# Kernel tuning notes

Measured on AMD Instinct MI355X. Metric: run time of the kernel, lower is better.

## Reference

```python
import jax, jax.numpy as jnp
import numpy as np

SCALE = 2

def pixel_shuffle(x, r):
    # x: (B, C*r*r, H, W) -> (B, C, H*r, W*r), torch F.pixel_shuffle ordering
    B, C, H, W = x.shape
    Co = C // (r * r)
    x = x.reshape(B, Co, r, r, H, W)
    x = x.transpose(0, 1, 4, 2, 5, 3)  # (B, Co, H, r, W, r)
    return x.reshape(B, Co, H * r, W * r)

def grid_sample_bilinear_zeros(x, grid):
    # x: (B,C,H,W); grid: (B,Ho,Wo,2), grid[...,0]=x-coord, grid[...,1]=y-coord
    # mode='bilinear', padding_mode='zeros', align_corners=False
    B, C, H, W = x.shape
    ix = ((grid[..., 0] + 1.0) * W - 1.0) * 0.5
    iy = ((grid[..., 1] + 1.0) * H - 1.0) * 0.5
    ix0 = jnp.floor(ix)
    iy0 = jnp.floor(iy)
    wx1 = ix - ix0
    wy1 = iy - iy0
    img = x.transpose(0, 2, 3, 1)  # (B,H,W,C) for channel-contiguous gathers
    b = jnp.arange(B)[:, None, None]

    def corner(iy_, ix_, w):
        valid = (ix_ >= 0) & (ix_ < W) & (iy_ >= 0) & (iy_ < H)
        ic = jnp.clip(ix_, 0, W - 1).astype(jnp.int32)
        jc = jnp.clip(iy_, 0, H - 1).astype(jnp.int32)
        v = img[b, jc, ic]  # (B,Ho,Wo,C)
        return v * (w * valid)[..., None]

    out = (corner(iy0, ix0, (1 - wy1) * (1 - wx1))
           + corner(iy0, ix0 + 1, (1 - wy1) * wx1)
           + corner(iy0 + 1, ix0, wy1 * (1 - wx1))
           + corner(iy0 + 1, ix0 + 1, wy1 * wx1))
    return out.transpose(0, 3, 1, 2)  # (B,C,Ho,Wo)

def setup_inputs() -> dict:
    key = jax.random.key(0)
    k1, k2, k3 = jax.random.split(key, 3)
    B, C, H, W = 16, 256, 64, 64
    x = jax.random.normal(k1, (B, C, H, W), dtype=jnp.float32)
    # 1x1 conv: weight (2*scale^2, C); original inits to zero, small random
    # values used here to exercise the learned-offset sampling path.
    weight = jax.random.normal(k2, (2 * SCALE * SCALE, C), dtype=jnp.float32) * 0.01
    bias = jax.random.normal(k3, (2 * SCALE * SCALE,), dtype=jnp.float32) * 0.01
    return {"x": x, "weight": weight, "bias": bias}

def reference(x, weight, bias):
    r = SCALE
    B, C, H, W = x.shape
    # 1x1 conv producing 2*r*r offset channels
    offset = jnp.einsum('bchw,oc->bohw', x, weight) + bias[None, :, None, None]
    offset = pixel_shuffle(offset, r)  # (B, 2, H*r, W*r)
    h_range = jnp.linspace(-1.0, 1.0, H * r, dtype=x.dtype)
    w_range = jnp.linspace(-1.0, 1.0, W * r, dtype=x.dtype)
    gh, gw = jnp.meshgrid(h_range, w_range, indexing='ij')
    # NOTE: original stacks (h, w) but grid_sample reads [...,0] as x-coord;
    # we reproduce that behavior exactly.
    grid = jnp.stack([gh, gw], axis=-1)[None]  # (1, Hr, Wr, 2)
    grid = grid + offset.transpose(0, 2, 3, 1)  # (B, Hr, Wr, 2)
    return grid_sample_bilinear_zeros(x, grid)
```

## Files before the change

### kernel.cpp

```cpp
#include <hip/hip_runtime.h>
#include <hip/hip_bf16.h>


#define NB 16
#define NC 256
#define NH 64
#define NW 64
#define NHO 128
#define NWO 128
#define PLANE (NH*NW)
#define OPLANE (NHO*NWO)

static __device__ __forceinline__ float bf2f(unsigned short u) {
    return __uint_as_float(((unsigned int)u) << 16);
}
static __device__ __forceinline__ unsigned short f2bf(float f) {
    unsigned int u = __float_as_uint(f);
    u = (u + 0x7FFFu + ((u >> 16) & 1u)) >> 16;
    return (unsigned short)u;
}
static __device__ __forceinline__ uint4 pack8(const float* r) {
    uint4 u;
    u.x = (unsigned)f2bf(r[0]) | ((unsigned)f2bf(r[1]) << 16);
    u.y = (unsigned)f2bf(r[2]) | ((unsigned)f2bf(r[3]) << 16);
    u.z = (unsigned)f2bf(r[4]) | ((unsigned)f2bf(r[5]) << 16);
    u.w = (unsigned)f2bf(r[6]) | ((unsigned)f2bf(r[7]) << 16);
    return u;
}

__global__ void k_detect(const unsigned int* __restrict__ xw, int* __restrict__ flag)
{
    __shared__ int cnt;
    if (threadIdx.x == 0) cnt = 0;
    __syncthreads();
    unsigned int w = xw[threadIdx.x];
    int el = (int)((w >> 7)  & 0xFFu);
    int eh = (int)((w >> 23) & 0xFFu);
    bool ok = (el >= 97 && el <= 143) && (eh >= 97 && eh <= 143);
    if (ok) atomicAdd(&cnt, 1);
    __syncthreads();
    if (threadIdx.x == 0) *flag = (cnt >= 192) ? 1 : 0;
}

__global__ __launch_bounds__(128) void k_offsets(
    const void* __restrict__ x_,
    const void* __restrict__ w_,
    const void* __restrict__ b_,
    float2* __restrict__ coords,
    const int* __restrict__ flag)
{
    __shared__ float4 wl4[NC * 2];
    float* wl = (float*)wl4;
    const int tid = threadIdx.x;
    const int isbf = *flag;

    if (isbf) {
        const unsigned short* weight = (const unsigned short*)w_;
        #pragma unroll
        for (int i = 0; i < 16; ++i) {
            int idx = tid * 16 + i;
            int c = idx >> 3, o = idx & 7;
            wl[idx] = bf2f(weight[o * NC + c]);
        }
    } else {
        const float* weight = (const float*)w_;
        #pragma unroll
        for (int i = 0; i < 16; ++i) {
            int idx = tid * 16 + i;
            int c = idx >> 3, o = idx & 7;
            wl[idx] = weight[o * NC + c];
        }
    }
    __syncthreads();

    float bv[8];
    if (isbf) {
        const unsigned short* bias = (const unsigned short*)b_;
        #pragma unroll
        for (int o = 0; o < 8; ++o) bv[o] = bf2f(bias[o]);
    } else {
        const float* bias = (const float*)b_;
        #pragma unroll
        for (int o = 0; o < 8; ++o) bv[o] = bias[o];
    }

    const int p0 = blockIdx.x * 256 + tid;
    const int p1 = p0 + 128;
    const int b0 = p0 >> 12, h0 = (p0 >> 6) & 63, w0 = p0 & 63;
    const int b1 = p1 >> 12, h1 = (p1 >> 6) & 63, w1 = p1 & 63;
    const size_t off0 = (size_t)b0 * NC * PLANE + h0 * NW + w0;
    const size_t off1 = (size_t)b1 * NC * PLANE + h1 * NW + w1;

    float a0[8], a1[8];
    #pragma unroll
    for (int o = 0; o < 8; ++o) { a0[o] = 0.0f; a1[o] = 0.0f; }

    if (isbf) {
        const unsigned short* xp0 = (const unsigned short*)x_ + off0;
        const unsigned short* xp1 = (const unsigned short*)x_ + off1;
        #pragma unroll 4
        for (int c = 0; c < NC; ++c) {
            float4 wA = wl4[c * 2], wB = wl4[c * 2 + 1];
            float wv[8] = { wA.x, wA.y, wA.z, wA.w, wB.x, wB.y, wB.z, wB.w };
            float xv0 = bf2f(xp0[c * PLANE]);
            float xv1 = bf2f(xp1[c * PLANE]);
            #pragma unroll
            for (int o = 0; o < 8; ++o) {
                a0[o] = fmaf(xv0, wv[o], a0[o]);
                a1[o] = fmaf(xv1, wv[o], a1[o]);
            }
        }
    } else {
        const float* xp0 = (const float*)x_ + off0;
        const float* xp1 = (const float*)x_ + off1;
        #pragma unroll 4
        for (int c = 0; c < NC; ++c) {
            float4 wA = wl4[c * 2], wB = wl4[c * 2 + 1];
            float wv[8] = { wA.x, wA.y, wA.z, wA.w, wB.x, wB.y, wB.z, wB.w };
            float xv0 = xp0[c * PLANE];
            float xv1 = xp1[c * PLANE];
            #pragma unroll
            for (int o = 0; o < 8; ++o) {
                a0[o] = fmaf(xv0, wv[o], a0[o]);
                a1[o] = fmaf(xv1, wv[o], a1[o]);
            }
        }
    }
    #pragma unroll
    for (int o = 0; o < 8; ++o) { a0[o] += bv[o]; a1[o] += bv[o]; }

    #pragma unroll
    for (int ry = 0; ry < 2; ++ry) {
        #pragma unroll
        for (int rx = 0; rx < 2; ++rx) {
            int q = ry * 2 + rx;
            {
                int ho = 2 * h0 + ry, wo = 2 * w0 + rx;
                float gh = fmaf((float)ho, 2.0f / 127.0f, -1.0f);
                float gw = fmaf((float)wo, 2.0f / 127.0f, -1.0f);
                float ix = ((gh + a0[q] + 1.0f) * 64.0f - 1.0f) * 0.5f;
                float iy = ((gw + a0[q + 4] + 1.0f) * 64.0f - 1.0f) * 0.5f;
                coords[(size_t)b0 * OPLANE + ho * NWO + wo] = make_float2(ix, iy);
            }
            {
                int ho = 2 * h1 + ry, wo = 2 * w1 + rx;
                float gh = fmaf((float)ho, 2.0f / 127.0f, -1.0f);
                float gw = fmaf((float)wo, 2.0f / 127.0f, -1.0f);
                float ix = ((gh + a1[q] + 1.0f) * 64.0f - 1.0f) * 0.5f;
                float iy = ((gw + a1[q + 4] + 1.0f) * 64.0f - 1.0f) * 0.5f;
                coords[(size_t)b1 * OPLANE + ho * NWO + wo] = make_float2(ix, iy);
            }
        }
    }
}

__global__ __launch_bounds__(256) void k_sample(
    const void* __restrict__ x_,
    const float2* __restrict__ coords,
    void* __restrict__ out_,
    const int* __restrict__ flag)
{
    __shared__ float4 plane[PLANE];
    const int tid = threadIdx.x;
    const int blk = blockIdx.x;
    const int g = blk & 63;
    const int b = blk >> 6;
    const int isbf = *flag;

    const size_t chbase = (size_t)(b * NC + g * 4) * PLANE;
    if (isbf) {
        const unsigned short* xb = (const unsigned short*)x_ + chbase;
        #pragma unroll
        for (int i = 0; i < 16; ++i) {
            int pos = i * 256 + tid;
            float4 v;
            v.x = bf2f(xb[pos]);
            v.y = bf2f(xb[PLANE + pos]);
            v.z = bf2f(xb[2 * PLANE + pos]);
            v.w = bf2f(xb[3 * PLANE + pos]);
            int y = pos >> 6;
            plane[(y << 6) | ((pos + (y >> 2)) & 63)] = v;
        }
    } else {
        const float* xb = (const float*)x_ + chbase;
        #pragma unroll
        for (int i = 0; i < 16; ++i) {
            int pos = i * 256 + tid;
            float4 v;
            v.x = xb[pos];
            v.y = xb[PLANE + pos];
            v.z = xb[2 * PLANE + pos];
            v.w = xb[3 * PLANE + pos];
            int y = pos >> 6;
            plane[(y << 6) | ((pos + (y >> 2)) & 63)] = v;
        }
    }
    __syncthreads();

    const float2* cb = coords + (size_t)b * OPLANE;
    const size_t obase = (size_t)(b * NC + g * 4) * OPLANE;

    #pragma unroll 1
    for (int it = 0; it < 8; ++it) {
        const int base = it * 2048 + tid * 8;
        float r0[8], r1[8], r2[8], r3[8];
        #pragma unroll
        for (int j = 0; j < 8; ++j) {
            float2 cd = cb[base + j];
            float ix = cd.x, iy = cd.y;
            float fx0 = floorf(ix), fy0 = floorf(iy);
            float wx1 = ix - fx0, wy1 = iy - fy0;
            float wx0 = 1.0f - wx1, wy0 = 1.0f - wy1;
            int x0 = (int)fx0, y0 = (int)fy0;
            int x1 = x0 + 1, y1 = y0 + 1;
            bool vx0 = (unsigned)x0 < 64u, vx1 = (unsigned)x1 < 64u;
            bool vy0 = (unsigned)y0 < 64u, vy1 = (unsigned)y1 < 64u;
            float w00 = (vy0 & vx0) ? wy0 * wx0 : 0.0f;
            float w01 = (vy0 & vx1) ? wy0 * wx1 : 0.0f;
            float w10 = (vy1 & vx0) ? wy1 * wx0 : 0.0f;
            float w11 = (vy1 & vx1) ? wy1 * wx1 : 0.0f;
            int x0c = min(max(x0, 0), 63), x1c = min(max(x1, 0), 63);
            int y0c = min(max(y0, 0), 63), y1c = min(max(y1, 0), 63);
            int ry0 = y0c >> 2, ry1 = y1c >> 2;
            float4 a00 = plane[(y0c << 6) | ((x0c + ry0) & 63)];
            float4 a01 = plane[(y0c << 6) | ((x1c + ry0) & 63)];
            float4 a10 = plane[(y1c << 6) | ((x0c + ry1) & 63)];
            float4 a11 = plane[(y1c << 6) | ((x1c + ry1) & 63)];
            r0[j] = w00 * a00.x + w01 * a01.x + w10 * a10.x + w11 * a11.x;
            r1[j] = w00 * a00.y + w01 * a01.y + w10 * a10.y + w11 * a11.y;
            r2[j] = w00 * a00.z + w01 * a01.z + w10 * a10.z + w11 * a11.z;
            r3[j] = w00 * a00.w + w01 * a01.w + w10 * a10.w + w11 * a11.w;
        }
        if (isbf) {
            unsigned short* ob = (unsigned short*)out_ + obase;
            *reinterpret_cast<uint4*>(ob + base)              = pack8(r0);
            *reinterpret_cast<uint4*>(ob + OPLANE + base)     = pack8(r1);
            *reinterpret_cast<uint4*>(ob + 2 * OPLANE + base) = pack8(r2);
            *reinterpret_cast<uint4*>(ob + 3 * OPLANE + base) = pack8(r3);
        } else {
            float* ob = (float*)out_ + obase;
            #pragma unroll
            for (int ch = 0; ch < 4; ++ch) {
                const float* rr = (ch == 0) ? r0 : (ch == 1) ? r1 : (ch == 2) ? r2 : r3;
                *reinterpret_cast<float4*>(ob + ch * OPLANE + base)     = make_float4(rr[0], rr[1], rr[2], rr[3]);
                *reinterpret_cast<float4*>(ob + ch * OPLANE + base + 4) = make_float4(rr[4], rr[5], rr[6], rr[7]);
            }
        }
    }
}

extern "C" void kernel_launch(void* const* d_in, const int* in_sizes, int n_in,
                              void* d_out, int out_size, void* d_ws, size_t ws_size,
                              hipStream_t stream)
{
    int* flag = (int*)d_ws;
    float2* coords = (float2*)((char*)d_ws + 256);

    hipLaunchKernelGGL(k_detect, dim3(1), dim3(256), 0, stream,
                       (const unsigned int*)d_in[0], flag);
    hipLaunchKernelGGL(k_offsets, dim3(256), dim3(128), 0, stream,
                       d_in[0], d_in[1], d_in[2], coords, flag);
    hipLaunchKernelGGL(k_sample, dim3(NB * 64), dim3(256), 0, stream,
                       d_in[0], coords, d_out, flag);
}
```

Baseline: 358.9 us.

## Drop dtype detection, split channel reduction across warps, widen sampling blocks

Removes the bf16 detection kernel and all bf16 branches, so x, weight and bias are assumed to be fp32. The offset conv now runs one block per output row, splits the 256 input channels across four waves and combines the partial sums in shared memory, then writes coordinates as float4. The sampling kernel goes to 512 threads, drops the LDS bank-swizzle, reads two coordinates per float4 and writes float2 outputs. This cuts a launch and raises parallelism in the conv, at the cost of possible LDS bank conflicts on the gathers and narrower output stores.

```diff
diff --git a/kernel.cpp b/kernel.cpp
--- a/kernel.cpp
+++ b/kernel.cpp
@@ -1,5 +1,4 @@
 #include <hip/hip_runtime.h>
-#include <hip/hip_bf16.h>
 
 
 #define NB 16
@@ -11,241 +10,145 @@
 #define PLANE (NH*NW)
 #define OPLANE (NHO*NWO)
 
-static __device__ __forceinline__ float bf2f(unsigned short u) {
-    return __uint_as_float(((unsigned int)u) << 16);
-}
-static __device__ __forceinline__ unsigned short f2bf(float f) {
-    unsigned int u = __float_as_uint(f);
-    u = (u + 0x7FFFu + ((u >> 16) & 1u)) >> 16;
-    return (unsigned short)u;
-}
-static __device__ __forceinline__ uint4 pack8(const float* r) {
-    uint4 u;
-    u.x = (unsigned)f2bf(r[0]) | ((unsigned)f2bf(r[1]) << 16);
-    u.y = (unsigned)f2bf(r[2]) | ((unsigned)f2bf(r[3]) << 16);
-    u.z = (unsigned)f2bf(r[4]) | ((unsigned)f2bf(r[5]) << 16);
-    u.w = (unsigned)f2bf(r[6]) | ((unsigned)f2bf(r[7]) << 16);
-    return u;
-}
-
-__global__ void k_detect(const unsigned int* __restrict__ xw, int* __restrict__ flag)
-{
-    __shared__ int cnt;
-    if (threadIdx.x == 0) cnt = 0;
-    __syncthreads();
-    unsigned int w = xw[threadIdx.x];
-    int el = (int)((w >> 7)  & 0xFFu);
-    int eh = (int)((w >> 23) & 0xFFu);
-    bool ok = (el >= 97 && el <= 143) && (eh >= 97 && eh <= 143);
-    if (ok) atomicAdd(&cnt, 1);
-    __syncthreads();
-    if (threadIdx.x == 0) *flag = (cnt >= 192) ? 1 : 0;
-}
-
-__global__ __launch_bounds__(128) void k_offsets(
-    const void* __restrict__ x_,
-    const void* __restrict__ w_,
-    const void* __restrict__ b_,
-    float2* __restrict__ coords,
-    const int* __restrict__ flag)
+__global__ __launch_bounds__(256, 4) void k_offsets(
+    const float* __restrict__ x,
+    const float* __restrict__ weight,
+    const float* __restrict__ bias,
+    float2* __restrict__ coords)
 {
     __shared__ float4 wl4[NC * 2];
+    __shared__ float red[4][64][8];
     float* wl = (float*)wl4;
     const int tid = threadIdx.x;
-    const int isbf = *flag;
+    const int qid = tid >> 6, w = tid & 63;
+    const int row = blockIdx.x;
+    const int b = row >> 6, h = row & 63;
 
-    if (isbf) {
-        const unsigned short* weight = (const unsigned short*)w_;
-        #pragma unroll
-        for (int i = 0; i < 16; ++i) {
-            int idx = tid * 16 + i;
-            int c = idx >> 3, o = idx & 7;
-            wl[idx] = bf2f(weight[o * NC + c]);
-        }
-    } else {
-        const float* weight = (const float*)w_;
-        #pragma unroll
-        for (int i = 0; i < 16; ++i) {
-            int idx = tid * 16 + i;
-            int c = idx >> 3, o = idx & 7;
-            wl[idx] = weight[o * NC + c];
-        }
+    #pragma unroll
+    for (int i = 0; i < 8; ++i) {
+        int idx = tid * 8 + i;
+        wl[idx] = weight[(idx & 7) * NC + (idx >> 3)];
     }
     __syncthreads();
 
-    float bv[8];
-    if (isbf) {
-        const unsigned short* bias = (const unsigned short*)b_;
-        #pragma unroll
-        for (int o = 0; o < 8; ++o) bv[o] = bf2f(bias[o]);
-    } else {
-        const float* bias = (const float*)b_;
-        #pragma unroll
-        for (int o = 0; o < 8; ++o) bv[o] = bias[o];
-    }
+    const float* xp = x + ((size_t)b * NC + (size_t)qid * 64) * PLANE + h * NW + w;
+    float acc[8];
+    #pragma unroll
+    for (int o = 0; o < 8; ++o) acc[o] = 0.0f;
 
-    const int p0 = blockIdx.x * 256 + tid;
-    const int p1 = p0 + 128;
-    const int b0 = p0 >> 12, h0 = (p0 >> 6) & 63, w0 = p0 & 63;
-    const int b1 = p1 >> 12, h1 = (p1 >> 6) & 63, w1 = p1 & 63;
-    const size_t off0 = (size_t)b0 * NC * PLANE + h0 * NW + w0;
-    const size_t off1 = (size_t)b1 * NC * PLANE + h1 * NW + w1;
-
-    float a0[8], a1[8];
-    #pragma unroll
-    for (int o = 0; o < 8; ++o) { a0[o] = 0.0f; a1[o] = 0.0f; }
-
-    if (isbf) {
-        const unsigned short* xp0 = (const unsigned short*)x_ + off0;
-        const unsigned short* xp1 = (const unsigned short*)x_ + off1;
-        #pragma unroll 4
-        for (int c = 0; c < NC; ++c) {
-            float4 wA = wl4[c * 2], wB = wl4[c * 2 + 1];
-            float wv[8] = { wA.x, wA.y, wA.z, wA.w, wB.x, wB.y, wB.z, wB.w };
-            float xv0 = bf2f(xp0[c * PLANE]);
-            float xv1 = bf2f(xp1[c * PLANE]);
-            #pragma unroll
-            for (int o = 0; o < 8; ++o) {
-                a0[o] = fmaf(xv0, wv[o], a0[o]);
-                a1[o] = fmaf(xv1, wv[o], a1[o]);
-            }
-        }
-    } else {
-        const float* xp0 = (const float*)x_ + off0;
-        const float* xp1 = (const float*)x_ + off1;
-        #pragma unroll 4
-        for (int c = 0; c < NC; ++c) {
-            float4 wA = wl4[c * 2], wB = wl4[c * 2 + 1];
-            float wv[8] = { wA.x, wA.y, wA.z, wA.w, wB.x, wB.y, wB.z, wB.w };
-            float xv0 = xp0[c * PLANE];
-            float xv1 = xp1[c * PLANE];
-            #pragma unroll
-            for (int o = 0; o < 8; ++o) {
-                a0[o] = fmaf(xv0, wv[o], a0[o]);
-                a1[o] = fmaf(xv1, wv[o], a1[o]);
-            }
-        }
+    #pragma unroll 8
+    for (int i = 0; i < 64; ++i) {
+        float xv = xp[(size_t)i * PLANE];
+        float4 wA = wl4[(qid * 64 + i) * 2];
+        float4 wB = wl4[(qid * 64 + i) * 2 + 1];
+        acc[0] = fmaf(xv, wA.x, acc[0]);
+        acc[1] = fmaf(xv, wA.y, acc[1]);
+        acc[2] = fmaf(xv, wA.z, acc[2]);
+        acc[3] = fmaf(xv, wA.w, acc[3]);
+        acc[4] = fmaf(xv, wB.x, acc[4]);
+        acc[5] = fmaf(xv, wB.y, acc[5]);
+        acc[6] = fmaf(xv, wB.z, acc[6]);
+        acc[7] = fmaf(xv, wB.w, acc[7]);
     }
     #pragma unroll
-    for (int o = 0; o < 8; ++o) { a0[o] += bv[o]; a1[o] += bv[o]; }
+    for (int o = 0; o < 8; ++o) red[qid][w][o] = acc[o];
+    __syncthreads();
 
-    #pragma unroll
-    for (int ry = 0; ry < 2; ++ry) {
+    if (tid < 64) {
+        float s[8];
         #pragma unroll
-        for (int rx = 0; rx < 2; ++rx) {
-            int q = ry * 2 + rx;
+        for (int o = 0; o < 8; ++o)
+            s[o] = red[0][tid][o] + red[1][tid][o] + red[2][tid][o] + red[3][tid][o]
+                 + bias[o];
+        float2* cb = coords + (size_t)b * OPLANE;
+        #pragma unroll
+        for (int ry = 0; ry < 2; ++ry) {
+            int ho = 2 * h + ry;
+            float gh = fmaf((float)ho, 2.0f / 127.0f, -1.0f);
+            float4 st;
             {
-                int ho = 2 * h0 + ry, wo = 2 * w0 + rx;
-                float gh = fmaf((float)ho, 2.0f / 127.0f, -1.0f);
+                int wo = 2 * tid;
                 float gw = fmaf((float)wo, 2.0f / 127.0f, -1.0f);
-                float ix = ((gh + a0[q] + 1.0f) * 64.0f - 1.0f) * 0.5f;
-                float iy = ((gw + a0[q + 4] + 1.0f) * 64.0f - 1.0f) * 0.5f;
-                coords[(size_t)b0 * OPLANE + ho * NWO + wo] = make_float2(ix, iy);
+                int q = ry * 2;
+                st.x = ((gh + s[q] + 1.0f) * 64.0f - 1.0f) * 0.5f;
+                st.y = ((gw + s[q + 4] + 1.0f) * 64.0f - 1.0f) * 0.5f;
             }
             {
-                int ho = 2 * h1 + ry, wo = 2 * w1 + rx;
-                float gh = fmaf((float)ho, 2.0f / 127.0f, -1.0f);
+                int wo = 2 * tid + 1;
                 float gw = fmaf((float)wo, 2.0f / 127.0f, -1.0f);
-                float ix = ((gh + a1[q] + 1.0f) * 64.0f - 1.0f) * 0.5f;
-                float iy = ((gw + a1[q + 4] + 1.0f) * 64.0f - 1.0f) * 0.5f;
-                coords[(size_t)b1 * OPLANE + ho * NWO + wo] = make_float2(ix, iy);
+                int q = ry * 2 + 1;
+                st.z = ((gh + s[q] + 1.0f) * 64.0f - 1.0f) * 0.5f;
+                st.w = ((gw + s[q + 4] + 1.0f) * 64.0f - 1.0f) * 0.5f;
             }
+            *reinterpret_cast<float4*>(cb + ho * NWO + 2 * tid) = st;
         }
     }
 }
 
-__global__ __launch_bounds__(256) void k_sample(
-    const void* __restrict__ x_,
+static __device__ __forceinline__ float4 samp4(const float4* __restrict__ plane,
+                                               float ix, float iy)
+{
+    float fx0 = floorf(ix), fy0 = floorf(iy);
+    float wx1 = ix - fx0, wy1 = iy - fy0;
+    float wx0 = 1.0f - wx1, wy0 = 1.0f - wy1;
+    int x0 = (int)fx0, y0 = (int)fy0;
+    int x1 = x0 + 1, y1 = y0 + 1;
+    bool vx0 = (unsigned)x0 < 64u, vx1 = (unsigned)x1 < 64u;
+    bool vy0 = (unsigned)y0 < 64u, vy1 = (unsigned)y1 < 64u;
+    float w00 = (vy0 & vx0) ? wy0 * wx0 : 0.0f;
+    float w01 = (vy0 & vx1) ? wy0 * wx1 : 0.0f;
+    float w10 = (vy1 & vx0) ? wy1 * wx0 : 0.0f;
+    float w11 = (vy1 & vx1) ? wy1 * wx1 : 0.0f;
+    int x0c = min(max(x0, 0), 63), x1c = min(max(x1, 0), 63);
+    int y0c = min(max(y0, 0), 63), y1c = min(max(y1, 0), 63);
+    float4 a00 = plane[(y0c << 6) | x0c];
+    float4 a01 = plane[(y0c << 6) | x1c];
+    float4 a10 = plane[(y1c << 6) | x0c];
+    float4 a11 = plane[(y1c << 6) | x1c];
+    float4 r;
+    r.x = w00 * a00.x + w01 * a01.x + w10 * a10.x + w11 * a11.x;
+    r.y = w00 * a00.y + w01 * a01.y + w10 * a10.y + w11 * a11.y;
+    r.z = w00 * a00.z + w01 * a01.z + w10 * a10.z + w11 * a11.z;
+    r.w = w00 * a00.w + w01 * a01.w + w10 * a10.w + w11 * a11.w;
+    return r;
+}
+
+__global__ __launch_bounds__(512, 4) void k_sample(
+    const float* __restrict__ x,
     const float2* __restrict__ coords,
-    void* __restrict__ out_,
-    const int* __restrict__ flag)
+    float* __restrict__ out)
 {
     __shared__ float4 plane[PLANE];
     const int tid = threadIdx.x;
-    const int blk = blockIdx.x;
-    const int g = blk & 63;
-    const int b = blk >> 6;
-    const int isbf = *flag;
+    const int g = blockIdx.x & 63;
+    const int b = blockIdx.x >> 6;
 
-    const size_t chbase = (size_t)(b * NC + g * 4) * PLANE;
-    if (isbf) {
-        const unsigned short* xb = (const unsigned short*)x_ + chbase;
-        #pragma unroll
-        for (int i = 0; i < 16; ++i) {
-            int pos = i * 256 + tid;
-            float4 v;
-            v.x = bf2f(xb[pos]);
-            v.y = bf2f(xb[PLANE + pos]);
-            v.z = bf2f(xb[2 * PLANE + pos]);
-            v.w = bf2f(xb[3 * PLANE + pos]);
-            int y = pos >> 6;
-            plane[(y << 6) | ((pos + (y >> 2)) & 63)] = v;
-        }
-    } else {
-        const float* xb = (const float*)x_ + chbase;
-        #pragma unroll
-        for (int i = 0; i < 16; ++i) {
-            int pos = i * 256 + tid;
-            float4 v;
-            v.x = xb[pos];
-            v.y = xb[PLANE + pos];
-            v.z = xb[2 * PLANE + pos];
-            v.w = xb[3 * PLANE + pos];
-            int y = pos >> 6;
-            plane[(y << 6) | ((pos + (y >> 2)) & 63)] = v;
-        }
+    const float* xb = x + ((size_t)(b * NC + g * 4)) * PLANE;
+    #pragma unroll
+    for (int i = 0; i < 8; ++i) {
+        int pos = i * 512 + tid;
+        float4 v;
+        v.x = xb[pos];
+        v.y = xb[PLANE + pos];
+        v.z = xb[2 * PLANE + pos];
+        v.w = xb[3 * PLANE + pos];
+        plane[pos] = v;
     }
     __syncthreads();
 
-    const float2* cb = coords + (size_t)b * OPLANE;
-    const size_t obase = (size_t)(b * NC + g * 4) * OPLANE;
+    const float4* cb4 = (const float4*)(coords + (size_t)b * OPLANE);
+    float* ob = out + ((size_t)(b * NC + g * 4)) * OPLANE;
 
     #pragma unroll 1
-    for (int it = 0; it < 8; ++it) {
-        const int base = it * 2048 + tid * 8;
-        float r0[8], r1[8], r2[8], r3[8];
-        #pragma unroll
-        for (int j = 0; j < 8; ++j) {
-            float2 cd = cb[base + j];
-            float ix = cd.x, iy = cd.y;
-            float fx0 = floorf(ix), fy0 = floorf(iy);
-            float wx1 = ix - fx0, wy1 = iy - fy0;
-            float wx0 = 1.0f - wx1, wy0 = 1.0f - wy1;
-            int x0 = (int)fx0, y0 = (int)fy0;
-            int x1 = x0 + 1, y1 = y0 + 1;
-            bool vx0 = (unsigned)x0 < 64u, vx1 = (unsigned)x1 < 64u;
-            bool vy0 = (unsigned)y0 < 64u, vy1 = (unsigned)y1 < 64u;
-            float w00 = (vy0 & vx0) ? wy0 * wx0 : 0.0f;
-            float w01 = (vy0 & vx1) ? wy0 * wx1 : 0.0f;
-            float w10 = (vy1 & vx0) ? wy1 * wx0 : 0.0f;
-            float w11 = (vy1 & vx1) ? wy1 * wx1 : 0.0f;
-            int x0c = min(max(x0, 0), 63), x1c = min(max(x1, 0), 63);
-            int y0c = min(max(y0, 0), 63), y1c = min(max(y1, 0), 63);
-            int ry0 = y0c >> 2, ry1 = y1c >> 2;
-            float4 a00 = plane[(y0c << 6) | ((x0c + ry0) & 63)];
-            float4 a01 = plane[(y0c << 6) | ((x1c + ry0) & 63)];
-            float4 a10 = plane[(y1c << 6) | ((x0c + ry1) & 63)];
-            float4 a11 = plane[(y1c << 6) | ((x1c + ry1) & 63)];
-            r0[j] = w00 * a00.x + w01 * a01.x + w10 * a10.x + w11 * a11.x;
-            r1[j] = w00 * a00.y + w01 * a01.y + w10 * a10.y + w11 * a11.y;
-            r2[j] = w00 * a00.z + w01 * a01.z + w10 * a10.z + w11 * a11.z;
-            r3[j] = w00 * a00.w + w01 * a01.w + w10 * a10.w + w11 * a11.w;
-        }
-        if (isbf) {
-            unsigned short* ob = (unsigned short*)out_ + obase;
-            *reinterpret_cast<uint4*>(ob + base)              = pack8(r0);
-            *reinterpret_cast<uint4*>(ob + OPLANE + base)     = pack8(r1);
-            *reinterpret_cast<uint4*>(ob + 2 * OPLANE + base) = pack8(r2);
-            *reinterpret_cast<uint4*>(ob + 3 * OPLANE + base) = pack8(r3);
-        } else {
-            float* ob = (float*)out_ + obase;
-            #pragma unroll
-            for (int ch = 0; ch < 4; ++ch) {
-                const float* rr = (ch == 0) ? r0 : (ch == 1) ? r1 : (ch == 2) ? r2 : r3;
-                *reinterpret_cast<float4*>(ob + ch * OPLANE + base)     = make_float4(rr[0], rr[1], rr[2], rr[3]);
-                *reinterpret_cast<float4*>(ob + ch * OPLANE + base + 4) = make_float4(rr[4], rr[5], rr[6], rr[7]);
-            }
-        }
+    for (int it = 0; it < 16; ++it) {
+        const int base = it * 1024 + tid * 2;
+        float4 cd = cb4[it * 512 + tid];
+        float4 p0 = samp4(plane, cd.x, cd.y);
+        float4 p1 = samp4(plane, cd.z, cd.w);
+        *reinterpret_cast<float2*>(ob + base)              = make_float2(p0.x, p1.x);
+        *reinterpret_cast<float2*>(ob + OPLANE + base)     = make_float2(p0.y, p1.y);
+        *reinterpret_cast<float2*>(ob + 2 * OPLANE + base) = make_float2(p0.z, p1.z);
+        *reinterpret_cast<float2*>(ob + 3 * OPLANE + base) = make_float2(p0.w, p1.w);
     }
 }
 
@@ -253,13 +156,14 @@
                               void* d_out, int out_size, void* d_ws, size_t ws_size,
                               hipStream_t stream)
 {
-    int* flag = (int*)d_ws;
-    float2* coords = (float2*)((char*)d_ws + 256);
+    const float* x      = (const float*)d_in[0];
+    const float* weight = (const float*)d_in[1];
+    const float* bias   = (const float*)d_in[2];
+    float* out = (float*)d_out;
+    float2* coords = (float2*)d_ws;
 
-    hipLaunchKernelGGL(k_detect, dim3(1), dim3(256), 0, stream,
-                       (const unsigned int*)d_in[0], flag);
-    hipLaunchKernelGGL(k_offsets, dim3(256), dim3(128), 0, stream,
-                       d_in[0], d_in[1], d_in[2], coords, flag);
-    hipLaunchKernelGGL(k_sample, dim3(NB * 64), dim3(256), 0, stream,
-                       d_in[0], coords, d_out, flag);
+    hipLaunchKernelGGL(k_offsets, dim3(NB * NH), dim3(256), 0, stream,
+                       x, weight, bias, coords);
+    hipLaunchKernelGGL(k_sample, dim3(NB * 64), dim3(512), 0, stream,
+                       x, coords, out);
 }
```

Result: faster. 337.7 us (-5.9%).
